# Performance work log

Measured on AMD Instinct MI355X. Metric: run time of the kernel, lower is better.

## Reference

```python
import jax, jax.numpy as jnp
import numpy as np
from functools import partial

IMG = 1024           # input image H = W
H_OUT = W_OUT = 64   # backbone feature map
SCALES = (64.0, 128.0, 256.0, 512.0)
RATIOS = (0.5, 1.0, 2.0)
A = len(SCALES) * len(RATIOS)          # 12 anchors per location
N_ANC = H_OUT * W_OUT * A              # 49152
PRENMS = 12000                          # hard-coded prenms_topn in source
TOP_N = 256
NMS_THRESH = 0.7
NEG = jnp.float32(-1e9)


def make_anchors():
    """Anchors in xyxy, grid order (h, w, anchor) to match permute(0,2,3,1).reshape."""
    stride_h = IMG / H_OUT
    stride_w = IMG / W_OUT
    cy = (np.arange(H_OUT, dtype=np.float32) + 0.5) * stride_h   # [H]
    cx = (np.arange(W_OUT, dtype=np.float32) + 0.5) * stride_w   # [W]
    ws, hs = [], []
    for s in SCALES:
        for r in RATIOS:
            ws.append(s * np.sqrt(r))
            hs.append(s / np.sqrt(r))
    ws = np.asarray(ws, np.float32)  # [A]
    hs = np.asarray(hs, np.float32)
    cy_g = cy[:, None, None]
    cx_g = cx[None, :, None]
    x1 = cx_g - ws / 2
    y1 = cy_g - hs / 2
    x2 = cx_g + ws / 2
    y2 = cy_g + hs / 2
    anc = np.stack(np.broadcast_arrays(x1, y1, x2, y2), axis=-1)  # [H,W,A,4]
    return jnp.asarray(anc.reshape(-1, 4))


def delta_to_boxes(deltas, anchors):
    """Standard R-CNN decoding. deltas [B,N,4], anchors [N,4] xyxy -> boxes xyxy."""
    wa = anchors[:, 2] - anchors[:, 0]
    ha = anchors[:, 3] - anchors[:, 1]
    cxa = anchors[:, 0] + 0.5 * wa
    cya = anchors[:, 1] + 0.5 * ha
    cx = deltas[..., 0] * wa + cxa
    cy = deltas[..., 1] * ha + cya
    w = wa * jnp.exp(deltas[..., 2])
    h = ha * jnp.exp(deltas[..., 3])
    return jnp.stack([cx - 0.5 * w, cy - 0.5 * h, cx + 0.5 * w, cy + 0.5 * h], axis=-1)


def iou_one_vs_all(box, boxes):
    x1 = jnp.maximum(box[0], boxes[:, 0])
    y1 = jnp.maximum(box[1], boxes[:, 1])
    x2 = jnp.minimum(box[2], boxes[:, 2])
    y2 = jnp.minimum(box[3], boxes[:, 3])
    inter = jnp.clip(x2 - x1, 0) * jnp.clip(y2 - y1, 0)
    area_a = (box[2] - box[0]) * (box[3] - box[1])
    area_b = (boxes[:, 2] - boxes[:, 0]) * (boxes[:, 3] - boxes[:, 1])
    return inter / (area_a + area_b - inter + 1e-7)


def nms_one(boxes, scores):
    """Greedy NMS, fixed TOP_N iterations. boxes [P,4], scores [P] -> [TOP_N,4]."""
    def body(i, carry):
        sel, sc = carry
        j = jnp.argmax(sc)
        best = boxes[j]
        valid = sc[j] > NEG * 0.5
        ious = iou_one_vs_all(best, boxes)
        sc = jnp.where(ious > NMS_THRESH, NEG, sc)  # also suppresses `best` itself
        sel = sel.at[i].set(jnp.where(valid, best, jnp.zeros(4, boxes.dtype)))
        return sel, sc
    sel0 = jnp.zeros((TOP_N, 4), boxes.dtype)
    sel, _ = jax.lax.fori_loop(0, TOP_N, body, (sel0, scores))
    return sel


def setup_inputs() -> dict:
    key = jax.random.key(0)
    ks = jax.random.split(key, 7)
    B, C, HID = 16, 512, 512
    return {
        "features": jax.random.normal(ks[0], (B, C, H_OUT, W_OUT), jnp.float32),
        "conv_w": jax.random.normal(ks[1], (HID, C, 3, 3), jnp.float32) * 0.01,
        "conv_b": jnp.zeros((HID,), jnp.float32),
        "reg_w": jax.random.normal(ks[2], (A * 4, HID), jnp.float32) * 0.01,
        "reg_b": jnp.zeros((A * 4,), jnp.float32),
        "conf_w": jax.random.normal(ks[3], (A, HID), jnp.float32) * 0.01,
        "conf_b": jnp.zeros((A,), jnp.float32),
    }


def reference(features, conv_w, conv_b, reg_w, reg_b, conf_w, conf_b):
    B = features.shape[0]
    anchors = make_anchors()                                   # [N,4]
    # proposal head: Conv3x3 -> (dropout=identity at inference) -> ReLU
    h = jax.lax.conv_general_dilated(
        features, conv_w, window_strides=(1, 1), padding="SAME",
        dimension_numbers=("NCHW", "OIHW", "NCHW"))
    h = jax.nn.relu(h + conv_b[None, :, None, None])            # [B,HID,H,W]
    # 1x1 heads, then permute(0,2,3,1).reshape as in source
    reg = jnp.einsum("bchw,oc->bhwo", h, reg_w) + reg_b         # [B,H,W,A*4]
    reg = reg.reshape(B, -1, 4)                                 # [B,N,4]
    conf = jnp.einsum("bchw,oc->bhwo", h, conf_w) + conf_b      # [B,H,W,A]
    conf = conf.reshape(B, -1)                                  # [B,N]

    boxes = delta_to_boxes(reg, anchors)                        # [B,N,4]
    top_conf, top_idx = jax.lax.top_k(conf, PRENMS)             # [B,P]
    top_boxes = jnp.take_along_axis(boxes, top_idx[..., None], axis=1)
    # clip boxes to image
    top_boxes = jnp.clip(top_boxes, 0.0, float(IMG))
    # size mask (degenerate boxes) -> kill score instead of filtering
    w = top_boxes[..., 2] - top_boxes[..., 0]
    hh = top_boxes[..., 3] - top_boxes[..., 1]
    top_conf = jnp.where((w >= 1.0) & (hh >= 1.0), top_conf, NEG)
    proposals = jax.vmap(nms_one)(top_boxes, top_conf)          # [B,TOP_N,4]
    return proposals
```

## Files before the change

### kernel.cpp

```cpp
#include <hip/hip_runtime.h>
#include <math.h>

#define NEGD (-1000000000.0)

typedef __attribute__((ext_vector_type(4))) double d4;
typedef __attribute__((ext_vector_type(2))) double d2;

__global__ void convert_w64(const float* __restrict__ w, double* __restrict__ w64)
{
    int i = blockIdx.x * 1024 + threadIdx.x;
    if (i < 2359296) w64[i] = (double)w[i];
}

__global__ void make_wT(const float* __restrict__ reg_w,
                        const float* __restrict__ conf_w,
                        double* __restrict__ wT)
{
    int i = blockIdx.x * 256 + threadIdx.x;
    if (i >= 512 * 64) return;
    int c = i >> 6, o = i & 63;
    double v = 0.0;
    if (o < 48)      v = (double)reg_w[o * 512 + c];
    else if (o < 60) v = (double)conf_w[(o - 48) * 512 + c];
    wT[i] = v;
}

__global__ __launch_bounds__(256, 4) void conv3x3_mfma_f64(
    const float* __restrict__ f, const double* __restrict__ w64,
    const float* __restrict__ bias, double* __restrict__ h, int b0)
{
    __shared__ double Xs[8 * 264];
    __shared__ double Ws[32 * 74];
    const int bl   = blockIdx.z;
    const int b    = b0 + bl;
    const int oc0  = blockIdx.y * 32;
    const int y0   = blockIdx.x * 2;
    const int tid  = threadIdx.x;
    const int wv   = tid >> 6;
    const int lane = tid & 63;
    const int fk   = lane >> 4;
    const int fm   = lane & 15;
    const int ryo  = wv >> 1;
    const int xb0  = (wv & 1) * 32;

    d4 zz = {0.0, 0.0, 0.0, 0.0};
    d4 p1 = __builtin_amdgcn_mfma_f64_16x16x4f64((double)fm, 1.0, zz, 0, 0, 0);
    d4 p2 = __builtin_amdgcn_mfma_f64_16x16x4f64(1.0, (double)fm, zz, 0, 0, 0);
    int ocl[4], pxl[4];
#pragma unroll
    for (int r = 0; r < 4; ++r) {
        ocl[r] = (int)(p1[r] * 0.25);
        pxl[r] = (int)(p2[r] * 0.25);
    }

    d4 a00 = zz, a01 = zz, a10 = zz, a11 = zz;

    for (int ic0 = 0; ic0 < 512; ic0 += 8) {
        for (int e = tid; e < 2112; e += 256) {
            int ic = e / 264, r = e - ic * 264;
            int ry = r / 66, cx = r - ry * 66;
            int gy = y0 + ry - 1, gx = cx - 1;
            double v = 0.0;
            if ((unsigned)gy < 64u && (unsigned)gx < 64u)
                v = (double)f[((b * 512 + ic0 + ic) * 64 + gy) * 64 + gx];
            Xs[e] = v;
        }
        for (int e = tid; e < 1152; e += 256) {
            int oc = e / 36, jj = (e - oc * 36) * 2;
            d2 v = *(const d2*)&w64[(size_t)(oc0 + oc) * 4608 + ic0 * 9 + jj];
            *(d2*)&Ws[oc * 74 + jj] = v;
        }
        __syncthreads();

#pragma unroll
        for (int s = 0; s < 2; ++s) {
            const int ick = s * 4 + fk;
            const double* xr  = &Xs[ick * 264 + ryo * 66 + xb0 + fm];
            const double* wr0 = &Ws[fm * 74 + ick * 9];
            const double* wr1 = &Ws[(fm + 16) * 74 + ick * 9];
#pragma unroll
            for (int ky = 0; ky < 3; ++ky) {
#pragma unroll
                for (int kx = 0; kx < 3; ++kx) {
                    double a0v = wr0[ky * 3 + kx];
                    double a1v = wr1[ky * 3 + kx];
                    double b0v = xr[ky * 66 + kx];
                    double b1v = xr[ky * 66 + kx + 16];
                    a00 = __builtin_amdgcn_mfma_f64_16x16x4f64(a0v, b0v, a00, 0, 0, 0);
                    a01 = __builtin_amdgcn_mfma_f64_16x16x4f64(a0v, b1v, a01, 0, 0, 0);
                    a10 = __builtin_amdgcn_mfma_f64_16x16x4f64(a1v, b0v, a10, 0, 0, 0);
                    a11 = __builtin_amdgcn_mfma_f64_16x16x4f64(a1v, b1v, a11, 0, 0, 0);
                }
            }
        }
        __syncthreads();
    }

    const int y = y0 + ryo;
#pragma unroll
    for (int r = 0; r < 4; ++r) {
        int ocA = oc0 + ocl[r];
        int ocB = oc0 + 16 + ocl[r];
        int px0 = xb0 + pxl[r];
        double bzA = (double)bias[ocA];
        double bzB = (double)bias[ocB];
        double v00 = a00[r] + bzA; v00 = v00 > 0.0 ? v00 : 0.0;
        double v01 = a01[r] + bzA; v01 = v01 > 0.0 ? v01 : 0.0;
        double v10 = a10[r] + bzB; v10 = v10 > 0.0 ? v10 : 0.0;
        double v11 = a11[r] + bzB; v11 = v11 > 0.0 ? v11 : 0.0;
        double* hA = &h[(((long)bl * 512 + ocA) * 64 + y) * 64];
        double* hB = &h[(((long)bl * 512 + ocB) * 64 + y) * 64];
        hA[px0]      = v00;
        hA[px0 + 16] = v01;
        hB[px0]      = v10;
        hB[px0 + 16] = v11;
    }
}

__global__ __launch_bounds__(256) void head_gemm_f64(
    const double* __restrict__ h, const double* __restrict__ wT,
    const float* __restrict__ reg_b, const float* __restrict__ conf_b,
    double* __restrict__ rc, int b0)
{
    __shared__ double h_t[32 * 128];
    __shared__ double w_t[32 * 64];
    const int bl  = blockIdx.y;
    const int b   = b0 + bl;
    const int hw0 = blockIdx.x * 128;
    const int tid = threadIdx.x;
    const int to  = tid >> 4;
    const int tp  = tid & 15;

    double acc[8][4];
#pragma unroll
    for (int j = 0; j < 8; ++j)
#pragma unroll
        for (int k = 0; k < 4; ++k) acc[j][k] = 0.0;

    for (int c0 = 0; c0 < 512; c0 += 32) {
        for (int e = tid; e < 32 * 128; e += 256) {
            int c = e >> 7, p = e & 127;
            h_t[e] = h[(bl * 512 + c0 + c) * 4096 + hw0 + p];
        }
        for (int e = tid; e < 32 * 64; e += 256) {
            w_t[e] = wT[(c0 + (e >> 6)) * 64 + (e & 63)];
        }
        __syncthreads();
#pragma unroll 4
        for (int c = 0; c < 32; ++c) {
            double wa[4], hv[8];
#pragma unroll
            for (int k = 0; k < 4; ++k) wa[k] = w_t[c * 64 + to * 4 + k];
#pragma unroll
            for (int j = 0; j < 8; ++j) hv[j] = h_t[c * 128 + tp * 8 + j];
#pragma unroll
            for (int j = 0; j < 8; ++j)
#pragma unroll
                for (int k = 0; k < 4; ++k)
                    acc[j][k] = fma(hv[j], wa[k], acc[j][k]);
        }
        __syncthreads();
    }
#pragma unroll
    for (int k = 0; k < 4; ++k) {
        int o = to * 4 + k;
        double bz = (o < 48) ? (double)reg_b[o] : (o < 60 ? (double)conf_b[o - 48] : 0.0);
#pragma unroll
        for (int j = 0; j < 8; ++j) acc[j][k] += bz;
    }
#pragma unroll
    for (int j = 0; j < 8; ++j)
#pragma unroll
        for (int k = 0; k < 4; ++k)
            rc[(long)(b * 4096 + hw0 + tp * 8 + j) * 64 + to * 4 + k] = acc[j][k];
}

__global__ void decode_f64(const double* __restrict__ rc,
                           double* __restrict__ boxes,
                           double* __restrict__ craw,
                           double* __restrict__ nsc)
{
    int g = blockIdx.x * 256 + threadIdx.x;
    if (g >= 16 * 49152) return;
    int b = g / 49152, n = g - b * 49152;
    int hw = n / 12, a = n - hw * 12;
    int y = hw >> 6, x = hw & 63;
    int si = a / 3, ri = a - si * 3;

    double s  = (double)(64 << si);
    double sr = (ri == 0) ? 0.70710678118654752440
              : (ri == 1) ? 1.0 : 1.41421356237309504880;
    float aw = (float)(s * sr);
    float ah = (float)(s / sr);

    float cyc = ((float)y + 0.5f) * 16.f;
    float cxc = ((float)x + 0.5f) * 16.f;
    float ax1 = cxc - aw * 0.5f;
    float ay1 = cyc - ah * 0.5f;
    float ax2 = cxc + aw * 0.5f;
    float ay2 = cyc + ah * 0.5f;

    double wa  = (double)ax2 - (double)ax1;
    double ha  = (double)ay2 - (double)ay1;
    double cxa = (double)ax1 + 0.5 * wa;
    double cya = (double)ay1 + 0.5 * ha;

    const double* r = rc + (long)(b * 4096 + hw) * 64;
    double d0 = r[a * 4 + 0];
    double d1 = r[a * 4 + 1];
    double d2v = r[a * 4 + 2];
    double d3 = r[a * 4 + 3];
    double conf = r[48 + a];

    double pcx = d0 * wa + cxa;
    double pcy = d1 * ha + cya;
    double pw  = wa * exp(d2v);
    double ph  = ha * exp(d3);

    double bx1 = pcx - 0.5 * pw;
    double by1 = pcy - 0.5 * ph;
    double bx2 = pcx + 0.5 * pw;
    double by2 = pcy + 0.5 * ph;

    bx1 = fmin(fmax(bx1, 0.0), 1024.0);
    by1 = fmin(fmax(by1, 0.0), 1024.0);
    bx2 = fmin(fmax(bx2, 0.0), 1024.0);
    by2 = fmin(fmax(by2, 0.0), 1024.0);

    double ww = bx2 - bx1, hh = by2 - by1;
    bool valid = (ww >= 1.0) && (hh >= 1.0);

    double* bo = boxes + (long)g * 4;
    bo[0] = bx1; bo[1] = by1; bo[2] = bx2; bo[3] = by2;
    craw[g] = conf;
    nsc[g]  = valid ? conf : NEGD;
}

__device__ __forceinline__ unsigned long long fkey64(double d) {
    unsigned long long u = (unsigned long long)__double_as_longlong(d);
    return (u & 0x8000000000000000ull) ? ~u : (u | 0x8000000000000000ull);
}

__global__ __launch_bounds__(1024) void topk_thresh64(
    const double* __restrict__ craw, unsigned long long* __restrict__ tinfo)
{
    __shared__ unsigned hist[256];
    __shared__ unsigned long long s_prefix;
    __shared__ int s_k;
    const int b = blockIdx.x, tid = threadIdx.x;
    const double* cb = craw + b * 49152;
    unsigned long long prefix = 0; int k = 12000;
    for (int pass = 0; pass < 8; ++pass) {
        const int shift = 56 - 8 * pass;
        if (tid < 256) hist[tid] = 0;
        __syncthreads();
        for (int i = tid; i < 49152; i += 1024) {
            unsigned long long u = fkey64(cb[i]);
            bool ok = (pass == 0) ||
                      ((u >> (shift + 8)) == (prefix >> (shift + 8)));
            if (ok) atomicAdd(&hist[(unsigned)(u >> shift) & 255u], 1u);
        }
        __syncthreads();
        if (tid == 0) {
            int kk = k, d = 0;
            for (int dd = 255; dd >= 0; --dd) {
                int c = (int)hist[dd];
                if (kk <= c) { d = dd; break; }
                kk -= c;
            }
            s_prefix = prefix | ((unsigned long long)d << shift);
            s_k = kk;
        }
        __syncthreads();
        prefix = s_prefix; k = s_k;
        __syncthreads();
    }
    if (tid == 0) { tinfo[b * 2] = prefix; tinfo[b * 2 + 1] = (unsigned long long)k; }
}

__global__ __launch_bounds__(1024) void compact_topk64(
    const double* __restrict__ craw, const double* __restrict__ boxes,
    const double* __restrict__ nsc, const unsigned long long* __restrict__ tinfo,
    double* __restrict__ cbox, double* __restrict__ csc)
{
    const int b = blockIdx.x, tid = threadIdx.x;
    const unsigned long long T = tinfo[b * 2];
    const unsigned E = (unsigned)tinfo[b * 2 + 1];
    const double* cb = craw + b * 49152;
    const int i0 = tid * 48;

    unsigned gt = 0, eq = 0;
    for (int j = 0; j < 48; ++j) {
        unsigned long long u = fkey64(cb[i0 + j]);
        gt += (u > T); eq += (u == T);
    }
    unsigned gi = gt, ei = eq;
    for (int d = 1; d < 64; d <<= 1) {
        unsigned g2 = __shfl_up(gi, d), e2 = __shfl_up(ei, d);
        if ((tid & 63) >= d) { gi += g2; ei += e2; }
    }
    __shared__ unsigned wg[16], we[16];
    if ((tid & 63) == 63) { wg[tid >> 6] = gi; we[tid >> 6] = ei; }
    __syncthreads();
    if (tid < 16) {
        unsigned a = wg[tid], c = we[tid];
        for (int d = 1; d < 16; d <<= 1) {
            unsigned a2 = __shfl_up(a, d), c2 = __shfl_up(c, d);
            if (tid >= d) { a += a2; c += c2; }
        }
        wg[tid] = a; we[tid] = c;
    }
    __syncthreads();
    unsigned g = gi - gt + ((tid >> 6) ? wg[(tid >> 6) - 1] : 0u);
    unsigned e = ei - eq + ((tid >> 6) ? we[(tid >> 6) - 1] : 0u);

    double* ob = cbox + (long)b * 12000 * 4;
    double* os = csc  + b * 12000;
    const double* bb = boxes + (long)b * 49152 * 4;
    const double* ns = nsc + b * 49152;
    for (int j = 0; j < 48; ++j) {
        int idx = i0 + j;
        unsigned long long u = fkey64(cb[idx]);
        if (u > T) {
            unsigned pos = g + (e < E ? e : E);
            ob[pos * 4 + 0] = bb[(long)idx * 4 + 0];
            ob[pos * 4 + 1] = bb[(long)idx * 4 + 1];
            ob[pos * 4 + 2] = bb[(long)idx * 4 + 2];
            ob[pos * 4 + 3] = bb[(long)idx * 4 + 3];
            os[pos] = ns[idx];
            ++g;
        } else if (u == T) {
            if (e < E) {
                unsigned pos = g + e;
                ob[pos * 4 + 0] = bb[(long)idx * 4 + 0];
                ob[pos * 4 + 1] = bb[(long)idx * 4 + 1];
                ob[pos * 4 + 2] = bb[(long)idx * 4 + 2];
                ob[pos * 4 + 3] = bb[(long)idx * 4 + 3];
                os[pos] = ns[idx];
            }
            ++e;
        }
    }
}

__global__ __launch_bounds__(1024) void nms64(
    const double* __restrict__ cbox, const double* __restrict__ csc,
    float* __restrict__ out)
{
    const int b = blockIdx.x, tid = threadIdx.x;
    const double* B4 = cbox + (long)b * 12000 * 4;
    const double* S  = csc  + b * 12000;

    double sc[12];
#pragma unroll
    for (int j = 0; j < 12; ++j) {
        int idx = tid + 1024 * j;
        sc[j] = (idx < 12000) ? S[idx] : NEGD;
    }

    __shared__ double wvv[16];
    __shared__ int    wii[16];
    float* O = out + b * 1024;

    for (int it = 0; it < 256; ++it) {
        double bv = sc[0]; int bj = 0;
#pragma unroll
        for (int j = 1; j < 12; ++j)
            if (sc[j] > bv) { bv = sc[j]; bj = j; }
        int bidx = tid + 1024 * bj;
        for (int d = 1; d < 64; d <<= 1) {
            double ov = __shfl_xor(bv, d);
            int    oi = __shfl_xor(bidx, d);
            if (ov > bv || (ov == bv && oi < bidx)) { bv = ov; bidx = oi; }
        }
        if ((tid & 63) == 0) { wvv[tid >> 6] = bv; wii[tid >> 6] = bidx; }
        __syncthreads();
        if (tid == 0) {
            double v = wvv[0]; int ix = wii[0];
            for (int q = 1; q < 16; ++q)
                if (wvv[q] > v || (wvv[q] == v && wii[q] < ix)) { v = wvv[q]; ix = wii[q]; }
            wvv[0] = v; wii[0] = ix;
        }
        __syncthreads();
        double bestv = wvv[0];
        int    besti = wii[0];
        const double* bb = B4 + (long)besti * 4;
        double b0 = bb[0], b1 = bb[1], b2 = bb[2], b3 = bb[3];
        bool valid = bestv > -5.0e8;
        if (tid == 0) {
            O[it * 4 + 0] = valid ? (float)b0 : 0.f;
            O[it * 4 + 1] = valid ? (float)b1 : 0.f;
            O[it * 4 + 2] = valid ? (float)b2 : 0.f;
            O[it * 4 + 3] = valid ? (float)b3 : 0.f;
        }
        double areaA = (b2 - b0) * (b3 - b1);
#pragma unroll
        for (int j = 0; j < 12; ++j) {
            if (sc[j] > -5.0e8) {
                int idx = tid + 1024 * j;
                const double* pb = B4 + (long)idx * 4;
                double x1 = fmax(b0, pb[0]);
                double y1 = fmax(b1, pb[1]);
                double x2 = fmin(b2, pb[2]);
                double y2 = fmin(b3, pb[3]);
                double iw = x2 - x1; iw = iw > 0.0 ? iw : 0.0;
                double ih = y2 - y1; ih = ih > 0.0 ? ih : 0.0;
                double inter = iw * ih;
                double areaB = (pb[2] - pb[0]) * (pb[3] - pb[1]);
                if (inter > 0.7 * (areaA + areaB - inter + 1e-7)) sc[j] = NEGD;
            }
        }
        __syncthreads();
    }
}

extern "C" void kernel_launch(void* const* d_in, const int* in_sizes, int n_in,
                              void* d_out, int out_size, void* d_ws, size_t ws_size,
                              hipStream_t stream)
{
    const float* f      = (const float*)d_in[0];
    const float* conv_w = (const float*)d_in[1];
    const float* conv_b = (const float*)d_in[2];
    const float* reg_w  = (const float*)d_in[3];
    const float* reg_b  = (const float*)d_in[4];
    const float* conf_w = (const float*)d_in[5];
    const float* conf_b = (const float*)d_in[6];

    double* ws = (double*)d_ws;
    double* wT    = ws;
    double* h     = ws + 32768;
    double* rc    = ws + 8421376;
    double* boxes = ws + 12615680;
    double* craw  = ws + 15761408;
    double* nsc   = ws + 16547840;
    double* cbox  = ws + 17334272;
    double* csc   = ws + 18102272;
    unsigned long long* tinfo = (unsigned long long*)(ws + 18294272);
    double* w64   = boxes;

    hipLaunchKernelGGL(convert_w64, dim3(2304), dim3(1024), 0, stream, conv_w, w64);
    hipLaunchKernelGGL(make_wT, dim3(128), dim3(256), 0, stream, reg_w, conf_w, wT);
    for (int q = 0; q < 4; ++q) {
        int b0 = q * 4;
        hipLaunchKernelGGL(conv3x3_mfma_f64, dim3(32, 16, 4), dim3(256), 0, stream,
                           f, w64, conv_b, h, b0);
        hipLaunchKernelGGL(head_gemm_f64, dim3(32, 4), dim3(256), 0, stream,
                           h, wT, reg_b, conf_b, rc, b0);
    }
    hipLaunchKernelGGL(decode_f64, dim3(3072), dim3(256), 0, stream,
                       rc, boxes, craw, nsc);
    hipLaunchKernelGGL(topk_thresh64, dim3(16), dim3(1024), 0, stream, craw, tinfo);
    hipLaunchKernelGGL(compact_topk64, dim3(16), dim3(1024), 0, stream,
                       craw, boxes, nsc, tinfo, cbox, csc);
    hipLaunchKernelGGL(nms64, dim3(16), dim3(1024), 0, stream,
                       cbox, csc, (float*)d_out);
}
```

Before: 8.490 ms.

## Double-buffer conv3x3 LDS tiles with register prefetch and transposed swizzled weights

Restructures the f64 MFMA 3x3 conv main loop to process 4 input channels per step with double-buffered shared memory. The next chunk is prefetched into registers while the current one is computed, so there is one barrier per iteration instead of two. Conv weights are pre-transposed to [c*9+tap][oc] so loads are coalesced across output channels, and the LDS layout uses an XOR-like rotation to avoid bank conflicts. The cost is more registers for prefetch, which could hurt occupancy under the 256x4 launch bounds.

Result: faster. 7.516 ms (-11.5%).

```diff
diff --git a/kernel.cpp b/kernel.cpp
--- a/kernel.cpp
+++ b/kernel.cpp
@@ -4,12 +4,13 @@
 #define NEGD (-1000000000.0)
 
 typedef __attribute__((ext_vector_type(4))) double d4;
-typedef __attribute__((ext_vector_type(2))) double d2;
-
-__global__ void convert_w64(const float* __restrict__ w, double* __restrict__ w64)
+
+__global__ void convert_w64t(const float* __restrict__ w, double* __restrict__ w64t)
 {
     int i = blockIdx.x * 1024 + threadIdx.x;
-    if (i < 2359296) w64[i] = (double)w[i];
+    if (i >= 2359296) return;
+    int c9t = i >> 9, oc = i & 511;
+    w64t[i] = (double)w[oc * 4608 + c9t];
 }
 
 __global__ void make_wT(const float* __restrict__ reg_w,
@@ -26,11 +27,11 @@
 }
 
 __global__ __launch_bounds__(256, 4) void conv3x3_mfma_f64(
-    const float* __restrict__ f, const double* __restrict__ w64,
+    const float* __restrict__ f, const double* __restrict__ w64t,
     const float* __restrict__ bias, double* __restrict__ h, int b0)
 {
-    __shared__ double Xs[8 * 264];
-    __shared__ double Ws[32 * 74];
+    __shared__ double Xs[2][1056];
+    __shared__ double Ws[2][1152];
     const int bl   = blockIdx.z;
     const int b    = b0 + bl;
     const int oc0  = blockIdx.y * 32;
@@ -42,6 +43,8 @@
     const int fm   = lane & 15;
     const int ryo  = wv >> 1;
     const int xb0  = (wv & 1) * 32;
+    const int c0r  = (fm + 8 * fk) & 31;
+    const int c1r  = (fm + 16 + 8 * fk) & 31;
 
     d4 zz = {0.0, 0.0, 0.0, 0.0};
     d4 p1 = __builtin_amdgcn_mfma_f64_16x16x4f64((double)fm, 1.0, zz, 0, 0, 0);
@@ -55,44 +58,72 @@
 
     d4 a00 = zz, a01 = zz, a10 = zz, a11 = zz;
 
-    for (int ic0 = 0; ic0 < 512; ic0 += 8) {
-        for (int e = tid; e < 2112; e += 256) {
-            int ic = e / 264, r = e - ic * 264;
-            int ry = r / 66, cx = r - ry * 66;
-            int gy = y0 + ry - 1, gx = cx - 1;
+    double xreg[5], wreg[5];
+
+    auto load_chunk = [&](int kc) {
+#pragma unroll
+        for (int i = 0; i < 5; ++i) {
+            int e = tid + 256 * i;
             double v = 0.0;
-            if ((unsigned)gy < 64u && (unsigned)gx < 64u)
-                v = (double)f[((b * 512 + ic0 + ic) * 64 + gy) * 64 + gx];
-            Xs[e] = v;
-        }
-        for (int e = tid; e < 1152; e += 256) {
-            int oc = e / 36, jj = (e - oc * 36) * 2;
-            d2 v = *(const d2*)&w64[(size_t)(oc0 + oc) * 4608 + ic0 * 9 + jj];
-            *(d2*)&Ws[oc * 74 + jj] = v;
-        }
-        __syncthreads();
-
-#pragma unroll
-        for (int s = 0; s < 2; ++s) {
-            const int ick = s * 4 + fk;
-            const double* xr  = &Xs[ick * 264 + ryo * 66 + xb0 + fm];
-            const double* wr0 = &Ws[fm * 74 + ick * 9];
-            const double* wr1 = &Ws[(fm + 16) * 74 + ick * 9];
-#pragma unroll
-            for (int ky = 0; ky < 3; ++ky) {
-#pragma unroll
-                for (int kx = 0; kx < 3; ++kx) {
-                    double a0v = wr0[ky * 3 + kx];
-                    double a1v = wr1[ky * 3 + kx];
-                    double b0v = xr[ky * 66 + kx];
-                    double b1v = xr[ky * 66 + kx + 16];
-                    a00 = __builtin_amdgcn_mfma_f64_16x16x4f64(a0v, b0v, a00, 0, 0, 0);
-                    a01 = __builtin_amdgcn_mfma_f64_16x16x4f64(a0v, b1v, a01, 0, 0, 0);
-                    a10 = __builtin_amdgcn_mfma_f64_16x16x4f64(a1v, b0v, a10, 0, 0, 0);
-                    a11 = __builtin_amdgcn_mfma_f64_16x16x4f64(a1v, b1v, a11, 0, 0, 0);
-                }
-            }
-        }
+            if (e < 1056) {
+                int ic = e / 264, r = e - ic * 264;
+                int ry = r / 66, cx = r - ry * 66;
+                int gy = y0 + ry - 1, gx = cx - 1;
+                if ((unsigned)gy < 64u && (unsigned)gx < 64u)
+                    v = (double)f[((b * 512 + kc * 4 + ic) * 64 + gy) * 64 + gx];
+            }
+            xreg[i] = v;
+        }
+#pragma unroll
+        for (int i = 0; i < 5; ++i) {
+            int e = tid + 256 * i;
+            if (e < 1152) {
+                int j = e >> 5, oc = e & 31;
+                wreg[i] = w64t[(size_t)(kc * 36 + j) * 512 + oc0 + oc];
+            }
+        }
+    };
+    auto write_chunk = [&](int buf) {
+#pragma unroll
+        for (int i = 0; i < 5; ++i) {
+            int e = tid + 256 * i;
+            if (e < 1056) Xs[buf][e] = xreg[i];
+        }
+#pragma unroll
+        for (int i = 0; i < 5; ++i) {
+            int e = tid + 256 * i;
+            if (e < 1152) {
+                int j = e >> 5, oc = e & 31;
+                Ws[buf][j * 32 + ((oc + 8 * (j / 9)) & 31)] = wreg[i];
+            }
+        }
+    };
+    auto compute_chunk = [&](int buf) {
+        const double* Xb = &Xs[buf][fk * 264 + ryo * 66 + xb0 + fm];
+        const double* Wb = &Ws[buf][fk * 288];
+#pragma unroll
+        for (int t = 0; t < 9; ++t) {
+            const int ky = t / 3, kx = t - ky * 3;
+            double a0v = Wb[t * 32 + c0r];
+            double a1v = Wb[t * 32 + c1r];
+            double b0v = Xb[ky * 66 + kx];
+            double b1v = Xb[ky * 66 + kx + 16];
+            a00 = __builtin_amdgcn_mfma_f64_16x16x4f64(a0v, b0v, a00, 0, 0, 0);
+            a01 = __builtin_amdgcn_mfma_f64_16x16x4f64(a0v, b1v, a01, 0, 0, 0);
+            a10 = __builtin_amdgcn_mfma_f64_16x16x4f64(a1v, b0v, a10, 0, 0, 0);
+            a11 = __builtin_amdgcn_mfma_f64_16x16x4f64(a1v, b1v, a11, 0, 0, 0);
+        }
+    };
+
+    load_chunk(0);
+    write_chunk(0);
+    __syncthreads();
+
+    for (int k = 0; k < 128; ++k) {
+        const int cur = k & 1;
+        if (k < 127) load_chunk(k + 1);
+        compute_chunk(cur);
+        if (k < 127) write_chunk(cur ^ 1);
         __syncthreads();
     }
 
@@ -436,14 +467,14 @@
     double* cbox  = ws + 17334272;
     double* csc   = ws + 18102272;
     unsigned long long* tinfo = (unsigned long long*)(ws + 18294272);
-    double* w64   = boxes;
-
-    hipLaunchKernelGGL(convert_w64, dim3(2304), dim3(1024), 0, stream, conv_w, w64);
+    double* w64t  = boxes;
+
+    hipLaunchKernelGGL(convert_w64t, dim3(2304), dim3(1024), 0, stream, conv_w, w64t);
     hipLaunchKernelGGL(make_wT, dim3(128), dim3(256), 0, stream, reg_w, conf_w, wT);
     for (int q = 0; q < 4; ++q) {
         int b0 = q * 4;
         hipLaunchKernelGGL(conv3x3_mfma_f64, dim3(32, 16, 4), dim3(256), 0, stream,
-                           f, w64, conv_b, h, b0);
+                           f, w64t, conv_b, h, b0);
         hipLaunchKernelGGL(head_gemm_f64, dim3(32, 4), dim3(256), 0, stream,
                            h, wT, reg_b, conf_b, rc, b0);
     }
```
